# Optimization experiments

Measured on AMD Instinct MI355X. Metric: run time of the kernel, lower is better.

## Reference

```python
import jax, jax.numpy as jnp
import numpy as np

K, D = 8, 4
LOG2PI = float(np.log(2.0 * np.pi))
TRIL_ROWS, TRIL_COLS = np.tril_indices(D)


def setup_inputs() -> dict:
    key = jax.random.key(0)
    k1, k2 = jax.random.split(key)
    M = 512
    B = 4096
    phi_dim = K + K * D + K * D * (D + 1) // 2  # 120
    phi = jax.random.normal(k1, (M, phi_dim), dtype=jnp.float32)
    X_ref = jax.random.normal(k2, (B, D), dtype=jnp.float32)
    return {"phi": phi, "X_ref": X_ref}


def reference(phi, X_ref):
    M = phi.shape[0]
    B = X_ref.shape[0]
    # unpack_phi: [pi_tilde | mu | L_vecs]
    pi_tilde = phi[:, :K]                                   # [M, K]
    mu = phi[:, K:K + K * D].reshape(M, K, D)               # [M, K, D]
    L_vecs = phi[:, K + K * D:].reshape(M, K, D * (D + 1) // 2)
    # L_vec_to_matrix: lower-triangular fill (row-major tril order)
    L = jnp.zeros((M, K, D, D), phi.dtype).at[:, :, TRIL_ROWS, TRIL_COLS].set(L_vecs)
    pi = jax.nn.softmax(pi_tilde, axis=-1)                  # [M, K]

    # --- mean responsibilities (GMM E-step) ---
    diff = X_ref[None, None, :, :] - mu[:, :, None, :]      # [M, K, B, D]
    L_flat = L.reshape(M * K, D, D)
    diff_flat = jnp.transpose(diff.reshape(M * K, B, D), (0, 2, 1))  # [MK, D, B]
    alpha = jax.scipy.linalg.solve_triangular(L_flat, diff_flat, lower=True)
    maha = (alpha ** 2).sum(1).reshape(M, K, B)             # Mahalanobis distances
    log_det = 2.0 * jnp.log(
        jnp.clip(jnp.abs(jnp.diagonal(L_flat, axis1=-2, axis2=-1)), 1e-8)
    ).sum(-1).reshape(M, K)
    log_norm = -0.5 * (D * LOG2PI + log_det[:, :, None])
    log_gauss = log_norm - 0.5 * maha                       # [M, K, B]
    log_joint = jnp.log(jnp.clip(pi, 1e-8))[:, :, None] + log_gauss
    log_resp = log_joint - jax.scipy.special.logsumexp(log_joint, axis=1, keepdims=True)
    resp = jnp.exp(log_resp).mean(-1)                       # [M, K]

    # --- combined embedding: [mu | log|diag L| | pi | resp] ---
    mu_flat = mu.reshape(M, K * D)
    L_diag = jnp.diagonal(L, axis1=-2, axis2=-1)            # [M, K, D]
    log_L_flat = jnp.log(jnp.clip(jnp.abs(L_diag), 1e-6)).reshape(M, K * D)
    z = jnp.concatenate([mu_flat, log_L_flat, pi, resp], axis=-1)

    # per-feature standardization across particles (torch.std => ddof=1)
    mean = z.mean(axis=0, keepdims=True)
    std = jnp.clip(z.std(axis=0, ddof=1, keepdims=True), 1e-6)
    return (z - mean) / std
```

## Files before the change

kernel.cpp:

```cpp
#include <hip/hip_runtime.h>
#include <math.h>

#define KK 8
#define LOG2E  1.4426950408889634f
#define HL2E   0.7213475204444817f
#define LOG2PI 1.8378770664093453f

__global__ __launch_bounds__(256) void gmm_main(const float* __restrict__ phi,
                                                const float* __restrict__ X,
                                                float* __restrict__ z) {
    __shared__ float4 sp[KK][4];
    __shared__ float swr[4][KK];

    const int b = blockIdx.x;
    const int m = b >> 2;
    const int sub = b & 3;
    const int t = threadIdx.x;
    const float* row = phi + m * 120;

    if (t < KK) {
        float mx = row[0];
        #pragma unroll
        for (int j = 1; j < KK; ++j) mx = fmaxf(mx, row[j]);
        float s = 0.f;
        #pragma unroll
        for (int j = 0; j < KK; ++j) s += __expf(row[j] - mx);
        float pik = __expf(row[t] - mx) / s;
        if (sub == 0) z[m * 80 + 64 + t] = pik;

        const float* muk = row + 8 + t * 4;
        const float* Lv  = row + 40 + t * 10;
        float l00 = Lv[0], l10 = Lv[1], l11 = Lv[2], l20 = Lv[3], l21 = Lv[4],
              l22 = Lv[5], l30 = Lv[6], l31 = Lv[7], l32 = Lv[8], l33 = Lv[9];
        float i0 = 1.f / l00, i1 = 1.f / l11, i2 = 1.f / l22, i3 = 1.f / l33;
        float w00 = i0;
        float w10 = -i1 * l10 * w00;
        float w11 = i1;
        float w20 = -i2 * (l20 * w00 + l21 * w10);
        float w21 = -i2 * (l21 * w11);
        float w22 = i2;
        float w30 = -i3 * (l30 * w00 + l31 * w10 + l32 * w20);
        float w31 = -i3 * (l31 * w11 + l32 * w21);
        float w32 = -i3 * (l32 * w22);
        float w33 = i3;
        float logdet = 2.f * (__logf(fmaxf(fabsf(l00), 1e-8f)) +
                              __logf(fmaxf(fabsf(l11), 1e-8f)) +
                              __logf(fmaxf(fabsf(l22), 1e-8f)) +
                              __logf(fmaxf(fabsf(l33), 1e-8f)));
        float c2 = (__logf(fmaxf(pik, 1e-8f)) -
                    0.5f * (4.f * LOG2PI + logdet)) * LOG2E;
        sp[t][0] = make_float4(muk[0], muk[1], muk[2], muk[3]);
        sp[t][1] = make_float4(w00, w10, w11, w20);
        sp[t][2] = make_float4(w21, w22, w30, w31);
        sp[t][3] = make_float4(w32, w33, c2, 0.f);
    } else if (sub == 0 && t >= 64 && t < 96) {
        int j = t - 64;
        z[m * 80 + j] = row[8 + j];
    } else if (sub == 0 && t >= 96 && t < 128) {
        int j = t - 96, k = j >> 2, d = j & 3;
        int didx = (d == 0) ? 0 : (d == 1) ? 2 : (d == 2) ? 5 : 9;
        z[m * 80 + 32 + j] = __logf(fmaxf(fabsf(row[40 + k * 10 + didx]), 1e-6f));
    }
    __syncthreads();

    float acc[KK];
    #pragma unroll
    for (int k = 0; k < KK; ++k) acc[k] = 0.f;

    const float4* X4 = reinterpret_cast<const float4*>(X);
    float4 xv[4];
    #pragma unroll
    for (int i = 0; i < 4; ++i) xv[i] = X4[sub * 1024 + i * 256 + t];

    float lj[4][KK];
    #pragma unroll
    for (int k = 0; k < KK; ++k) {
        float4 p0 = sp[k][0], p1 = sp[k][1], p2 = sp[k][2], p3 = sp[k][3];
        #pragma unroll
        for (int i = 0; i < 4; ++i) {
            float d0 = xv[i].x - p0.x;
            float d1 = xv[i].y - p0.y;
            float d2 = xv[i].z - p0.z;
            float d3 = xv[i].w - p0.w;
            float a0 = d0 * p1.x;
            float a1 = fmaf(p1.y, d0, d1 * p1.z);
            float a2 = fmaf(p1.w, d0, fmaf(p2.x, d1, d2 * p2.y));
            float a3 = fmaf(p2.z, d0, fmaf(p2.w, d1, fmaf(p3.x, d2, d3 * p3.y)));
            float sq = fmaf(a0, a0, fmaf(a1, a1, fmaf(a2, a2, a3 * a3)));
            lj[i][k] = fmaf(-HL2E, sq, p3.z);
        }
    }
    #pragma unroll
    for (int i = 0; i < 4; ++i) {
        float mx = lj[i][0];
        #pragma unroll
        for (int k = 1; k < KK; ++k) mx = fmaxf(mx, lj[i][k]);
        float e[KK], s = 0.f;
        #pragma unroll
        for (int k = 0; k < KK; ++k) {
            e[k] = __builtin_amdgcn_exp2f(lj[i][k] - mx);
            s += e[k];
        }
        float inv = __builtin_amdgcn_rcpf(s);
        #pragma unroll
        for (int k = 0; k < KK; ++k) acc[k] = fmaf(e[k], inv, acc[k]);
    }

    #pragma unroll
    for (int k = 0; k < KK; ++k) {
        float v = acc[k];
        #pragma unroll
        for (int off = 32; off; off >>= 1) v += __shfl_xor(v, off, 64);
        acc[k] = v;
    }
    if ((t & 63) == 0) {
        int wid = t >> 6;
        #pragma unroll
        for (int k = 0; k < KK; ++k) swr[wid][k] = acc[k];
    }
    __syncthreads();
    if (t < KK) {
        float s = swr[0][t] + swr[1][t] + swr[2][t] + swr[3][t];
        atomicAdd(&z[m * 80 + 72 + t], s);
    }
}

__global__ __launch_bounds__(512) void gmm_norm(float* __restrict__ z, int M) {
    __shared__ float sw[8];
    const int col = blockIdx.x;
    const int t = threadIdx.x;

    float v = z[t * 80 + col];

    float r = v;
    #pragma unroll
    for (int off = 32; off; off >>= 1) r += __shfl_xor(r, off, 64);
    if ((t & 63) == 0) sw[t >> 6] = r;
    __syncthreads();
    float tot = 0.f;
    #pragma unroll
    for (int w = 0; w < 8; ++w) tot += sw[w];
    float mean = tot / (float)M;
    __syncthreads();

    float d = v - mean;
    r = d * d;
    #pragma unroll
    for (int off = 32; off; off >>= 1) r += __shfl_xor(r, off, 64);
    if ((t & 63) == 0) sw[t >> 6] = r;
    __syncthreads();
    float tot2 = 0.f;
    #pragma unroll
    for (int w = 0; w < 8; ++w) tot2 += sw[w];
    float stdv = fmaxf(sqrtf(tot2 / (float)(M - 1)), 1e-6f);

    z[t * 80 + col] = d / stdv;
}

extern "C" void kernel_launch(void* const* d_in, const int* in_sizes, int n_in,
                              void* d_out, int out_size, void* d_ws, size_t ws_size,
                              hipStream_t stream) {
    const float* phi = (const float*)d_in[0];
    const float* X   = (const float*)d_in[1];
    const int M = in_sizes[0] / 120;
    float* z = (float*)d_out;

    hipMemsetAsync(z, 0, (size_t)out_size * sizeof(float), stream);
    gmm_main<<<M * 4, 256, 0, stream>>>(phi, X, z);
    gmm_norm<<<80, 512, 0, stream>>>(z, M);
}
```

Baseline: 71.35 us.

## Replace atomic resp accumulation with workspace partials reduced in norm kernel

Each wave now writes its eight per-component partial sums to a workspace buffer, and the normalization kernel sums the 16 partials per particle. This removes the second __syncthreads, the shared-memory reduction and the atomicAdds in the main kernel, and also drops the hipMemsetAsync on the output (one fewer launch). In exchange the norm kernel does strided workspace reads for the resp columns, and the result depends on the workspace being large enough.

```diff
diff --git a/kernel.cpp b/kernel.cpp
--- a/kernel.cpp
+++ b/kernel.cpp
@@ -8,9 +8,9 @@
 
 __global__ __launch_bounds__(256) void gmm_main(const float* __restrict__ phi,
                                                 const float* __restrict__ X,
-                                                float* __restrict__ z) {
+                                                float* __restrict__ z,
+                                                float* __restrict__ ws) {
     __shared__ float4 sp[KK][4];
-    __shared__ float swr[4][KK];
 
     const int b = blockIdx.x;
     const int m = b >> 2;
@@ -114,23 +114,30 @@
         acc[k] = v;
     }
     if ((t & 63) == 0) {
-        int wid = t >> 6;
-        #pragma unroll
-        for (int k = 0; k < KK; ++k) swr[wid][k] = acc[k];
-    }
-    __syncthreads();
-    if (t < KK) {
-        float s = swr[0][t] + swr[1][t] + swr[2][t] + swr[3][t];
-        atomicAdd(&z[m * 80 + 72 + t], s);
+        const int wid = t >> 6;
+        float* w = ws + ((size_t)b * 4 + wid) * 8;
+        reinterpret_cast<float4*>(w)[0] = make_float4(acc[0], acc[1], acc[2], acc[3]);
+        reinterpret_cast<float4*>(w)[1] = make_float4(acc[4], acc[5], acc[6], acc[7]);
     }
 }
 
-__global__ __launch_bounds__(512) void gmm_norm(float* __restrict__ z, int M) {
+__global__ __launch_bounds__(512) void gmm_norm(float* __restrict__ z,
+                                                const float* __restrict__ ws,
+                                                int M) {
     __shared__ float sw[8];
     const int col = blockIdx.x;
     const int t = threadIdx.x;
 
-    float v = z[t * 80 + col];
+    float v;
+    if (col >= 72) {
+        const float* w = ws + (size_t)t * 128 + (col - 72);
+        float s = 0.f;
+        #pragma unroll
+        for (int p = 0; p < 16; ++p) s += w[p * 8];
+        v = s;
+    } else {
+        v = z[t * 80 + col];
+    }
 
     float r = v;
     #pragma unroll
@@ -163,9 +170,9 @@
     const float* phi = (const float*)d_in[0];
     const float* X   = (const float*)d_in[1];
     const int M = in_sizes[0] / 120;
-    float* z = (float*)d_out;
+    float* z  = (float*)d_out;
+    float* ws = (float*)d_ws;
 
-    hipMemsetAsync(z, 0, (size_t)out_size * sizeof(float), stream);
-    gmm_main<<<M * 4, 256, 0, stream>>>(phi, X, z);
-    gmm_norm<<<80, 512, 0, stream>>>(z, M);
+    gmm_main<<<M * 4, 256, 0, stream>>>(phi, X, z, ws);
+    gmm_norm<<<80, 512, 0, stream>>>(z, ws, M);
 }
```

After: 73.35 us. 2.8% more time.
